# Optimization experiments

Hardware: AMD Instinct MI355X
Metric: run time of the kernel (lower is better)

Reference implementation:

```python
import jax, jax.numpy as jnp
import numpy as np

N = 100000   # num nodes
E = 500000   # num edges
F_IN = 128   # num_feats
H = 128      # dim_hidden
C = 40       # num_classes


def _glorot(key, fan_in, fan_out):
    lim = np.sqrt(6.0 / (fan_in + fan_out)).astype(np.float32)
    return jax.random.uniform(key, (fan_in, fan_out), jnp.float32, -lim, lim)


def setup_inputs() -> dict:
    key = jax.random.key(0)
    ks = jax.random.split(key, 8)
    x = jax.random.normal(ks[0], (N, F_IN), dtype=jnp.float32)
    edge_index = jax.random.randint(ks[1], (2, E), 0, N, dtype=jnp.int32)
    dims = [F_IN, H, H, H, C]  # num_layers = 4
    inp = {"x": x, "edge_index": edge_index}
    for i in range(4):
        inp[f"W{i}"] = _glorot(ks[2 + i], dims[i], dims[i + 1])
        inp[f"b{i}"] = jnp.zeros((dims[i + 1],), jnp.float32)
    return inp


def _gcn_norm(edge_index, num_nodes):
    # PyG gcn_norm: add self-loops (weight 1), symmetric D^-1/2 A D^-1/2
    loops = jnp.arange(num_nodes, dtype=edge_index.dtype)
    src = jnp.concatenate([edge_index[0], loops])
    dst = jnp.concatenate([edge_index[1], loops])
    deg = jax.ops.segment_sum(jnp.ones_like(src, jnp.float32), dst,
                              num_segments=num_nodes)
    dinv = jnp.where(deg > 0, jax.lax.rsqrt(deg), 0.0)
    norm = dinv[src] * dinv[dst]  # [E + N]
    return src, dst, norm


def _gcn_conv(h, W, b, src, dst, norm, num_nodes):
    h = h @ W                               # [N, out]
    msg = h[src] * norm[:, None]            # gather + scale, [E+N, out]
    agg = jax.ops.segment_sum(msg, dst, num_segments=num_nodes)
    return agg + b


def reference(x, edge_index, W0, b0, W1, b1, W2, b2, W3, b3):
    # eval mode: feature dropout and edge dropout (dropout_adj) are identity;
    # type_norm='None' -> no batchnorm.
    src, dst, norm = _gcn_norm(edge_index, N)
    Ws = [W0, W1, W2, W3]
    bs = [b0, b1, b2, b3]
    h = x
    for i in range(3):  # num_layers - 1 hidden layers with ReLU
        h = jax.nn.relu(_gcn_conv(h, Ws[i], bs[i], src, dst, norm, N))
    return _gcn_conv(h, Ws[3], bs[3], src, dst, norm, N)  # [N, C]
```

## Files before the change

### kernel.cpp

```cpp
#include <hip/hip_runtime.h>
#include <hip/hip_bf16.h>


#define F_DIM 128

#define SCAN_T 256
#define SCAN_I 8
#define SCAN_CHUNK (SCAN_T * SCAN_I)

typedef __attribute__((ext_vector_type(8))) short short8;
typedef __attribute__((ext_vector_type(4))) float f32x4;

__device__ __forceinline__ unsigned short f2bf_rne(float f) {
    unsigned int u = __float_as_uint(f);
    unsigned int r = (u + 0x7fffu + ((u >> 16) & 1u)) >> 16;
    return (unsigned short)r;
}

__global__ void count_dst_kernel(const int* __restrict__ dst, int* __restrict__ count, int E) {
    int e = blockIdx.x * blockDim.x + threadIdx.x;
    if (e < E) atomicAdd(&count[dst[e]], 1);
}

__global__ __launch_bounds__(SCAN_T) void scan_partial_kernel(const int* __restrict__ count,
                                                              int* __restrict__ blocksum, int n) {
    int b = blockIdx.x, t = threadIdx.x;
    int base = b * SCAN_CHUNK + t * SCAN_I;
    int s = 0;
#pragma unroll
    for (int j = 0; j < SCAN_I; ++j) {
        int i = base + j;
        if (i < n) s += count[i] + 1;
    }
    __shared__ int red[SCAN_T];
    red[t] = s;
    __syncthreads();
    for (int off = SCAN_T / 2; off > 0; off >>= 1) {
        if (t < off) red[t] += red[t + off];
        __syncthreads();
    }
    if (t == 0) blocksum[b] = red[0];
}

__global__ __launch_bounds__(1024) void scan_sums_kernel(const int* __restrict__ blocksum,
                                                         int* __restrict__ blockoff, int nb) {
    __shared__ int sums[1024];
    int t = threadIdx.x;
    sums[t] = (t < nb) ? blocksum[t] : 0;
    __syncthreads();
    for (int off = 1; off < 1024; off <<= 1) {
        int v = (t >= off) ? sums[t - off] : 0;
        __syncthreads();
        sums[t] += v;
        __syncthreads();
    }
    if (t < nb) blockoff[t] = (t == 0) ? 0 : sums[t - 1];
    if (t == 0) blockoff[nb] = sums[nb - 1];
}

__global__ __launch_bounds__(SCAN_T) void scan_write_fused_kernel(const int* __restrict__ count,
                                                                  const int* __restrict__ blockoff,
                                                                  int* __restrict__ rowptr,
                                                                  int* __restrict__ writepos,
                                                                  float* __restrict__ dinv,
                                                                  int* __restrict__ col,
                                                                  float* __restrict__ val,
                                                                  int n, int nb) {
    int b = blockIdx.x, t = threadIdx.x;
    int base = b * SCAN_CHUNK + t * SCAN_I;
    int c[SCAN_I];
    int s = 0;
#pragma unroll
    for (int j = 0; j < SCAN_I; ++j) {
        int i = base + j;
        c[j] = (i < n) ? count[i] + 1 : 0;
        s += c[j];
    }
    __shared__ int sums[SCAN_T];
    sums[t] = s;
    __syncthreads();
    for (int off = 1; off < SCAN_T; off <<= 1) {
        int v = (t >= off) ? sums[t - off] : 0;
        __syncthreads();
        sums[t] += v;
        __syncthreads();
    }
    int offset = blockoff[b] + ((t == 0) ? 0 : sums[t - 1]);
#pragma unroll
    for (int j = 0; j < SCAN_I; ++j) {
        int i = base + j;
        if (i < n) {
            rowptr[i] = offset;
            float d = rsqrtf((float)c[j]);
            dinv[i] = d;
            col[offset] = i;
            val[offset] = d * d;
            writepos[i] = offset + 1;
            offset += c[j];
        }
    }
    if (b == 0 && t == 0) rowptr[n] = blockoff[nb];
}

__global__ void fill_edges_kernel(const int* __restrict__ src, const int* __restrict__ dst,
                                  int* __restrict__ writepos, int* __restrict__ col,
                                  float* __restrict__ val, const float* __restrict__ dinv, int E) {
    int e = blockIdx.x * blockDim.x + threadIdx.x;
    if (e < E) {
        int s = src[e], d = dst[e];
        int p = atomicAdd(&writepos[d], 1);
        col[p] = s;
        val[p] = dinv[s] * dinv[d];
    }
}

__global__ __launch_bounds__(256) void cvt_bf16_kernel(const float* __restrict__ in,
                                                       unsigned short* __restrict__ out,
                                                       long nChunks) {
    long idx = (long)blockIdx.x * 256 + threadIdx.x;
    if (idx >= nChunks) return;
    const float4* in4 = (const float4*)in;
    float4 a = in4[idx * 2];
    float4 b = in4[idx * 2 + 1];
    uint4 o;
    o.x = (unsigned)f2bf_rne(a.x) | ((unsigned)f2bf_rne(a.y) << 16);
    o.y = (unsigned)f2bf_rne(a.z) | ((unsigned)f2bf_rne(a.w) << 16);
    o.z = (unsigned)f2bf_rne(b.x) | ((unsigned)f2bf_rne(b.y) << 16);
    o.w = (unsigned)f2bf_rne(b.z) | ((unsigned)f2bf_rne(b.w) << 16);
    ((uint4*)out)[idx] = o;
}

__global__ __launch_bounds__(256) void cvt_weights_kernel(const float* __restrict__ W0,
                                                          const float* __restrict__ W1,
                                                          const float* __restrict__ W2,
                                                          const float* __restrict__ W3,
                                                          unsigned short* __restrict__ WT0,
                                                          unsigned short* __restrict__ WT1,
                                                          unsigned short* __restrict__ WT2,
                                                          unsigned short* __restrict__ WT3) {
    int t = blockIdx.x * 256 + threadIdx.x;
    if (t < 3 * 16384) {
        int w = t >> 14, i = t & 16383;
        int k = i >> 7, c = i & 127;
        const float* W = (w == 0) ? W0 : (w == 1) ? W1 : W2;
        unsigned short* WT = (w == 0) ? WT0 : (w == 1) ? WT1 : WT2;
        WT[(size_t)c * 128 + k] = f2bf_rne(W[(size_t)k * 128 + c]);
    } else {
        int i = t - 3 * 16384;
        if (i < 48 * 128) {
            int c = i >> 7, k = i & 127;
            WT3[(size_t)c * 128 + k] = (c < 40) ? f2bf_rne(W3[(size_t)k * 40 + c])
                                                : (unsigned short)0;
        }
    }
}

__device__ __forceinline__ void acc8_bf16(float* acc, uint4 u, float v) {
    unsigned w[4] = {u.x, u.y, u.z, u.w};
#pragma unroll
    for (int i = 0; i < 4; ++i) {
        float lo = __uint_as_float(w[i] << 16);
        float hi = __uint_as_float(w[i] & 0xffff0000u);
        acc[2 * i] += v * lo;
        acc[2 * i + 1] += v * hi;
    }
}

__device__ __forceinline__ void gather_phase1(const int* __restrict__ rowptr,
                                              const int* __restrict__ col,
                                              const float* __restrict__ val,
                                              const uint4* __restrict__ H16,
                                              unsigned short (*aggb)[136], int n) {
    int m = threadIdx.x >> 3;
    int p = threadIdx.x & 7;
    int node = blockIdx.x * 32 + m;
    float acc[16];
#pragma unroll
    for (int q = 0; q < 16; ++q) acc[q] = 0.f;
    if (node < n) {
        int s = rowptr[node], e = rowptr[node + 1];
        int j = s;
        for (; j + 3 < e; j += 4) {
            int c0 = col[j], c1 = col[j + 1], c2 = col[j + 2], c3 = col[j + 3];
            float v0 = val[j], v1 = val[j + 1], v2 = val[j + 2], v3 = val[j + 3];
            const uint4* r0 = H16 + (size_t)c0 * 16 + p;
            const uint4* r1 = H16 + (size_t)c1 * 16 + p;
            const uint4* r2 = H16 + (size_t)c2 * 16 + p;
            const uint4* r3 = H16 + (size_t)c3 * 16 + p;
            uint4 a0 = r0[0], a1 = r0[8];
            uint4 b0 = r1[0], b1 = r1[8];
            uint4 g0 = r2[0], g1 = r2[8];
            uint4 d0 = r3[0], d1 = r3[8];
            acc8_bf16(acc + 0, a0, v0);
            acc8_bf16(acc + 8, a1, v0);
            acc8_bf16(acc + 0, b0, v1);
            acc8_bf16(acc + 8, b1, v1);
            acc8_bf16(acc + 0, g0, v2);
            acc8_bf16(acc + 8, g1, v2);
            acc8_bf16(acc + 0, d0, v3);
            acc8_bf16(acc + 8, d1, v3);
        }
        for (; j + 1 < e; j += 2) {
            int c0 = col[j], c1 = col[j + 1];
            float v0 = val[j], v1 = val[j + 1];
            const uint4* r0 = H16 + (size_t)c0 * 16 + p;
            const uint4* r1 = H16 + (size_t)c1 * 16 + p;
            uint4 a0 = r0[0], a1 = r0[8];
            uint4 b0 = r1[0], b1 = r1[8];
            acc8_bf16(acc + 0, a0, v0);
            acc8_bf16(acc + 8, a1, v0);
            acc8_bf16(acc + 0, b0, v1);
            acc8_bf16(acc + 8, b1, v1);
        }
        if (j < e) {
            int c0 = col[j];
            float v0 = val[j];
            const uint4* r0 = H16 + (size_t)c0 * 16 + p;
            uint4 a0 = r0[0], a1 = r0[8];
            acc8_bf16(acc + 0, a0, v0);
            acc8_bf16(acc + 8, a1, v0);
        }
    }
    short8 s0, s1;
#pragma unroll
    for (int q = 0; q < 8; ++q) s0[q] = (short)f2bf_rne(acc[q]);
#pragma unroll
    for (int q = 0; q < 8; ++q) s1[q] = (short)f2bf_rne(acc[8 + q]);
    *(short8*)&aggb[m][8 * p] = s0;
    *(short8*)&aggb[m][64 + 8 * p] = s1;
}

__global__ __launch_bounds__(256, 6) void fused_layer_mfma(const int* __restrict__ rowptr,
                                                           const int* __restrict__ col,
                                                           const float* __restrict__ val,
                                                           const unsigned short* __restrict__ Hin,
                                                           const unsigned short* __restrict__ WT,
                                                           const float* __restrict__ bias,
                                                           unsigned short* __restrict__ Hout,
                                                           int n) {
    __shared__ unsigned short aggb[32][136];
    gather_phase1(rowptr, col, val, (const uint4*)Hin, aggb, n);
    __syncthreads();

    int lane = threadIdx.x & 63;
    int wv = threadIdx.x >> 6;
    int l15 = lane & 15;
    int lg = lane >> 4;

    f32x4 a00 = {0.f, 0.f, 0.f, 0.f}, a01 = a00, a10 = a00, a11 = a00;

#pragma unroll
    for (int kc = 0; kc < 4; ++kc) {
        int ko = kc * 32 + lg * 8;
        short8 fa0 = *(const short8*)&aggb[l15][ko];
        short8 fa1 = *(const short8*)&aggb[l15 + 16][ko];
        short8 fb0 = *(const short8*)&WT[(size_t)(wv * 32 + l15) * 128 + ko];
        short8 fb1 = *(const short8*)&WT[(size_t)(wv * 32 + 16 + l15) * 128 + ko];
        a00 = __builtin_amdgcn_mfma_f32_16x16x32_bf16(fa0, fb0, a00, 0, 0, 0);
        a01 = __builtin_amdgcn_mfma_f32_16x16x32_bf16(fa0, fb1, a01, 0, 0, 0);
        a10 = __builtin_amdgcn_mfma_f32_16x16x32_bf16(fa1, fb0, a10, 0, 0, 0);
        a11 = __builtin_amdgcn_mfma_f32_16x16x32_bf16(fa1, fb1, a11, 0, 0, 0);
    }

    int base = blockIdx.x * 32;
#pragma unroll
    for (int nt = 0; nt < 2; ++nt) {
        int c = wv * 32 + nt * 16 + l15;
        float bv = bias[c];
#pragma unroll
        for (int mt = 0; mt < 2; ++mt) {
            f32x4 acc = (mt == 0) ? (nt == 0 ? a00 : a01) : (nt == 0 ? a10 : a11);
#pragma unroll
            for (int r = 0; r < 4; ++r) {
                int node = base + mt * 16 + lg * 4 + r;
                if (node < n) {
                    float o = fmaxf(acc[r] + bv, 0.f);
                    Hout[(size_t)node * 128 + c] = f2bf_rne(o);
                }
            }
        }
    }
}

__global__ __launch_bounds__(256, 6) void fused_layer_mfma_w3(const int* __restrict__ rowptr,
                                                              const int* __restrict__ col,
                                                              const float* __restrict__ val,
                                                              const unsigned short* __restrict__ Hin,
                                                              const unsigned short* __restrict__ WT,
                                                              const float* __restrict__ bias,
                                                              const unsigned short* __restrict__ WT3,
                                                              unsigned short* __restrict__ hw3,
                                                              int n) {
    __shared__ unsigned short aggb[32][136];
    gather_phase1(rowptr, col, val, (const uint4*)Hin, aggb, n);
    __syncthreads();

    int lane = threadIdx.x & 63;
    int wv = threadIdx.x >> 6;
    int l15 = lane & 15;
    int lg = lane >> 4;

    f32x4 a00 = {0.f, 0.f, 0.f, 0.f}, a01 = a00, a10 = a00, a11 = a00;

#pragma unroll
    for (int kc = 0; kc < 4; ++kc) {
        int ko = kc * 32 + lg * 8;
        short8 fa0 = *(const short8*)&aggb[l15][ko];
        short8 fa1 = *(const short8*)&aggb[l15 + 16][ko];
        short8 fb0 = *(const short8*)&WT[(size_t)(wv * 32 + l15) * 128 + ko];
        short8 fb1 = *(const short8*)&WT[(size_t)(wv * 32 + 16 + l15) * 128 + ko];
        a00 = __builtin_amdgcn_mfma_f32_16x16x32_bf16(fa0, fb0, a00, 0, 0, 0);
        a01 = __builtin_amdgcn_mfma_f32_16x16x32_bf16(fa0, fb1, a01, 0, 0, 0);
        a10 = __builtin_amdgcn_mfma_f32_16x16x32_bf16(fa1, fb0, a10, 0, 0, 0);
        a11 = __builtin_amdgcn_mfma_f32_16x16x32_bf16(fa1, fb1, a11, 0, 0, 0);
    }

    __syncthreads();
#pragma unroll
    for (int nt = 0; nt < 2; ++nt) {
        int c = wv * 32 + nt * 16 + l15;
        float bv = bias[c];
#pragma unroll
        for (int mt = 0; mt < 2; ++mt) {
            f32x4 acc = (mt == 0) ? (nt == 0 ? a00 : a01) : (nt == 0 ? a10 : a11);
#pragma unroll
            for (int r = 0; r < 4; ++r) {
                int row = mt * 16 + lg * 4 + r;
                aggb[row][c] = f2bf_rne(fmaxf(acc[r] + bv, 0.f));
            }
        }
    }
    __syncthreads();

    if (wv < 3) {
        f32x4 c0 = {0.f, 0.f, 0.f, 0.f}, c1 = c0;
#pragma unroll
        for (int kc = 0; kc < 4; ++kc) {
            int ko = kc * 32 + lg * 8;
            short8 fa0 = *(const short8*)&aggb[l15][ko];
            short8 fa1 = *(const short8*)&aggb[l15 + 16][ko];
            short8 fb = *(const short8*)&WT3[(size_t)(wv * 16 + l15) * 128 + ko];
            c0 = __builtin_amdgcn_mfma_f32_16x16x32_bf16(fa0, fb, c0, 0, 0, 0);
            c1 = __builtin_amdgcn_mfma_f32_16x16x32_bf16(fa1, fb, c1, 0, 0, 0);
        }
        int ccol = wv * 16 + l15;
        if (ccol < 40) {
            int base = blockIdx.x * 32;
#pragma unroll
            for (int mt = 0; mt < 2; ++mt) {
                f32x4 acc = (mt == 0) ? c0 : c1;
#pragma unroll
                for (int r = 0; r < 4; ++r) {
                    int node = base + mt * 16 + lg * 4 + r;
                    if (node < n) hw3[(size_t)node * 40 + ccol] = f2bf_rne(acc[r]);
                }
            }
        }
    }
}

__global__ __launch_bounds__(256, 8) void gather40_bf16_kernel(const int* __restrict__ rowptr,
                                                               const int* __restrict__ col,
                                                               const float* __restrict__ val,
                                                               const unsigned short* __restrict__ hw3,
                                                               const float* __restrict__ bias,
                                                               float* __restrict__ out, int n) {
    int m = threadIdx.x >> 3;
    int p = threadIdx.x & 7;
    int node = blockIdx.x * 32 + m;
    if (node >= n) return;

    float a0x = 0.f, a0y = 0.f, a0z = 0.f, a0w = 0.f;
    float a1x = 0.f, a1y = 0.f, a1z = 0.f, a1w = 0.f;

    int s = rowptr[node], e = rowptr[node + 1];
    int j = s;
    for (; j + 1 < e; j += 2) {
        int c0 = col[j], c1 = col[j + 1];
        float v0 = val[j], v1 = val[j + 1];
        const uint2* r0 = (const uint2*)(hw3 + (size_t)c0 * 40);
        const uint2* r1 = (const uint2*)(hw3 + (size_t)c1 * 40);
        uint2 u0 = r0[p], u1 = r1[p];
        a0x += v0 * __uint_as_float(u0.x << 16) + v1 * __uint_as_float(u1.x << 16);
        a0y += v0 * __uint_as_float(u0.x & 0xffff0000u) + v1 * __uint_as_float(u1.x & 0xffff0000u);
        a0z += v0 * __uint_as_float(u0.y << 16) + v1 * __uint_as_float(u1.y << 16);
        a0w += v0 * __uint_as_float(u0.y & 0xffff0000u) + v1 * __uint_as_float(u1.y & 0xffff0000u);
        if (p < 2) {
            uint2 w0 = r0[8 + p], w1 = r1[8 + p];
            a1x += v0 * __uint_as_float(w0.x << 16) + v1 * __uint_as_float(w1.x << 16);
            a1y += v0 * __uint_as_float(w0.x & 0xffff0000u) + v1 * __uint_as_float(w1.x & 0xffff0000u);
            a1z += v0 * __uint_as_float(w0.y << 16) + v1 * __uint_as_float(w1.y << 16);
            a1w += v0 * __uint_as_float(w0.y & 0xffff0000u) + v1 * __uint_as_float(w1.y & 0xffff0000u);
        }
    }
    if (j < e) {
        int c0 = col[j];
        float v0 = val[j];
        const uint2* r0 = (const uint2*)(hw3 + (size_t)c0 * 40);
        uint2 u = r0[p];
        a0x += v0 * __uint_as_float(u.x << 16);
        a0y += v0 * __uint_as_float(u.x & 0xffff0000u);
        a0z += v0 * __uint_as_float(u.y << 16);
        a0w += v0 * __uint_as_float(u.y & 0xffff0000u);
        if (p < 2) {
            uint2 w = r0[8 + p];
            a1x += v0 * __uint_as_float(w.x << 16);
            a1y += v0 * __uint_as_float(w.x & 0xffff0000u);
            a1z += v0 * __uint_as_float(w.y << 16);
            a1w += v0 * __uint_as_float(w.y & 0xffff0000u);
        }
    }

    const float4* bi = (const float4*)bias;
    float4 bv = bi[p];
    float4 o0;
    o0.x = a0x + bv.x; o0.y = a0y + bv.y;
    o0.z = a0z + bv.z; o0.w = a0w + bv.w;
    ((float4*)(out + (size_t)node * 40))[p] = o0;
    if (p < 2) {
        float4 bw = bi[8 + p];
        float4 o1;
        o1.x = a1x + bw.x; o1.y = a1y + bw.y;
        o1.z = a1z + bw.z; o1.w = a1w + bw.w;
        ((float4*)(out + (size_t)node * 40))[8 + p] = o1;
    }
}

extern "C" void kernel_launch(void* const* d_in, const int* in_sizes, int n_in,
                              void* d_out, int out_size, void* d_ws, size_t ws_size,
                              hipStream_t stream) {
    const float* x = (const float*)d_in[0];
    const int* edge_index = (const int*)d_in[1];
    const float* W0 = (const float*)d_in[2];
    const float* b0 = (const float*)d_in[3];
    const float* W1 = (const float*)d_in[4];
    const float* b1 = (const float*)d_in[5];
    const float* W2 = (const float*)d_in[6];
    const float* b2 = (const float*)d_in[7];
    const float* W3 = (const float*)d_in[8];
    const float* b3 = (const float*)d_in[9];

    const int E = in_sizes[1] / 2;
    const int N = in_sizes[0] / F_DIM;
    const int NNZ = E + N;
    const int NB = (N + SCAN_CHUNK - 1) / SCAN_CHUNK;

    const int* src = edge_index;
    const int* dst = edge_index + E;

    char* ws = (char*)d_ws;
    size_t off = 0;
    auto carve = [&](size_t bytes) -> void* {
        void* p = ws + off;
        off = (off + bytes + 255) & ~(size_t)255;
        return p;
    };
    unsigned short* hbA = (unsigned short*)carve((size_t)N * F_DIM * sizeof(unsigned short));
    unsigned short* hbB = (unsigned short*)carve((size_t)N * F_DIM * sizeof(unsigned short));
    unsigned short* hw3 = (unsigned short*)carve((size_t)N * 40 * sizeof(unsigned short));
    unsigned short* WT0 = (unsigned short*)carve(128 * 128 * sizeof(unsigned short));
    unsigned short* WT1 = (unsigned short*)carve(128 * 128 * sizeof(unsigned short));
    unsigned short* WT2 = (unsigned short*)carve(128 * 128 * sizeof(unsigned short));
    unsigned short* WT3 = (unsigned short*)carve(48 * 128 * sizeof(unsigned short));
    int* count = (int*)carve((size_t)N * sizeof(int));
    float* dinv = (float*)carve((size_t)N * sizeof(float));
    int* rowptr = (int*)carve((size_t)(N + 1) * sizeof(int));
    int* writepos = (int*)carve((size_t)N * sizeof(int));
    int* colbuf = (int*)carve((size_t)NNZ * sizeof(int));
    float* valbuf = (float*)carve((size_t)NNZ * sizeof(float));
    int* blocksum = (int*)carve((size_t)NB * sizeof(int));
    int* blockoff = (int*)carve((size_t)(NB + 1) * sizeof(int));
    (void)ws_size;

    hipMemsetAsync(count, 0, (size_t)N * sizeof(int), stream);
    count_dst_kernel<<<(E + 255) / 256, 256, 0, stream>>>(dst, count, E);
    {
        long nChunks = (long)N * F_DIM / 8;
        cvt_bf16_kernel<<<(int)((nChunks + 255) / 256), 256, 0, stream>>>(x, hbA, nChunks);
    }
    cvt_weights_kernel<<<(3 * 16384 + 48 * 128 + 255) / 256, 256, 0, stream>>>(
        W0, W1, W2, W3, WT0, WT1, WT2, WT3);
    scan_partial_kernel<<<NB, SCAN_T, 0, stream>>>(count, blocksum, N);
    scan_sums_kernel<<<1, 1024, 0, stream>>>(blocksum, blockoff, NB);
    scan_write_fused_kernel<<<NB, SCAN_T, 0, stream>>>(count, blockoff, rowptr, writepos,
                                                       dinv, colbuf, valbuf, N, NB);
    fill_edges_kernel<<<(E + 255) / 256, 256, 0, stream>>>(src, dst, writepos, colbuf, valbuf, dinv, E);

    int nblk32 = (N + 31) / 32;
    fused_layer_mfma<<<nblk32, 256, 0, stream>>>(rowptr, colbuf, valbuf, hbA, WT0, b0, hbB, N);
    fused_layer_mfma<<<nblk32, 256, 0, stream>>>(rowptr, colbuf, valbuf, hbB, WT1, b1, hbA, N);
    fused_layer_mfma_w3<<<nblk32, 256, 0, stream>>>(rowptr, colbuf, valbuf, hbA, WT2, b2, WT3, hw3, N);

    gather40_bf16_kernel<<<nblk32, 256, 0, stream>>>(rowptr, colbuf, valbuf, hw3, b3, (float*)d_out, N);
}
```

Measured before the change: 257.5 us.

## Merge preprocessing kernels, drop 4-way gather unroll, raise occupancy bound to 8

Three independent preprocessing kernels (degree counting, feature bf16 conversion, weight transpose/convert) are merged into one launch that picks its role from the block index, removing two launch gaps. The 4-edge unrolled gather loop is removed so the gather runs 2 edges at a time, and the launch-bounds minimum blocks per CU on the fused layer kernels rises from 6 to 8. Together these lower register pressure and raise occupancy, trading per-thread memory-level parallelism for more resident waves. The tighter register budget could also cause spills.

```diff
diff --git a/kernel.cpp b/kernel.cpp
--- a/kernel.cpp
+++ b/kernel.cpp
@@ -17,9 +17,54 @@
     return (unsigned short)r;
 }
 
-__global__ void count_dst_kernel(const int* __restrict__ dst, int* __restrict__ count, int E) {
-    int e = blockIdx.x * blockDim.x + threadIdx.x;
-    if (e < E) atomicAdd(&count[dst[e]], 1);
+__global__ __launch_bounds__(256) void preproc_kernel(const int* __restrict__ dst,
+                                                      int* __restrict__ count, int E,
+                                                      const float* __restrict__ x,
+                                                      unsigned short* __restrict__ xb,
+                                                      long nChunks,
+                                                      const float* __restrict__ W0,
+                                                      const float* __restrict__ W1,
+                                                      const float* __restrict__ W2,
+                                                      const float* __restrict__ W3,
+                                                      unsigned short* __restrict__ WT0,
+                                                      unsigned short* __restrict__ WT1,
+                                                      unsigned short* __restrict__ WT2,
+                                                      unsigned short* __restrict__ WT3,
+                                                      int EB, int XB) {
+    int b = blockIdx.x;
+    if (b < EB) {
+        int e = b * 256 + threadIdx.x;
+        if (e < E) atomicAdd(&count[dst[e]], 1);
+    } else if (b < EB + XB) {
+        long idx = (long)(b - EB) * 256 + threadIdx.x;
+        if (idx < nChunks) {
+            const float4* in4 = (const float4*)x;
+            float4 a = in4[idx * 2];
+            float4 c = in4[idx * 2 + 1];
+            uint4 o;
+            o.x = (unsigned)f2bf_rne(a.x) | ((unsigned)f2bf_rne(a.y) << 16);
+            o.y = (unsigned)f2bf_rne(a.z) | ((unsigned)f2bf_rne(a.w) << 16);
+            o.z = (unsigned)f2bf_rne(c.x) | ((unsigned)f2bf_rne(c.y) << 16);
+            o.w = (unsigned)f2bf_rne(c.z) | ((unsigned)f2bf_rne(c.w) << 16);
+            ((uint4*)xb)[idx] = o;
+        }
+    } else {
+        int t = (b - EB - XB) * 256 + threadIdx.x;
+        if (t < 3 * 16384) {
+            int w = t >> 14, i = t & 16383;
+            int k = i >> 7, c = i & 127;
+            const float* W = (w == 0) ? W0 : (w == 1) ? W1 : W2;
+            unsigned short* WT = (w == 0) ? WT0 : (w == 1) ? WT1 : WT2;
+            WT[(size_t)c * 128 + k] = f2bf_rne(W[(size_t)k * 128 + c]);
+        } else {
+            int i = t - 3 * 16384;
+            if (i < 48 * 128) {
+                int c = i >> 7, k = i & 127;
+                WT3[(size_t)c * 128 + k] = (c < 40) ? f2bf_rne(W3[(size_t)k * 40 + c])
+                                                    : (unsigned short)0;
+            }
+        }
+    }
 }
 
 __global__ __launch_bounds__(SCAN_T) void scan_partial_kernel(const int* __restrict__ count,
@@ -114,47 +159,6 @@
     }
 }
 
-__global__ __launch_bounds__(256) void cvt_bf16_kernel(const float* __restrict__ in,
-                                                       unsigned short* __restrict__ out,
-                                                       long nChunks) {
-    long idx = (long)blockIdx.x * 256 + threadIdx.x;
-    if (idx >= nChunks) return;
-    const float4* in4 = (const float4*)in;
-    float4 a = in4[idx * 2];
-    float4 b = in4[idx * 2 + 1];
-    uint4 o;
-    o.x = (unsigned)f2bf_rne(a.x) | ((unsigned)f2bf_rne(a.y) << 16);
-    o.y = (unsigned)f2bf_rne(a.z) | ((unsigned)f2bf_rne(a.w) << 16);
-    o.z = (unsigned)f2bf_rne(b.x) | ((unsigned)f2bf_rne(b.y) << 16);
-    o.w = (unsigned)f2bf_rne(b.z) | ((unsigned)f2bf_rne(b.w) << 16);
-    ((uint4*)out)[idx] = o;
-}
-
-__global__ __launch_bounds__(256) void cvt_weights_kernel(const float* __restrict__ W0,
-                                                          const float* __restrict__ W1,
-                                                          const float* __restrict__ W2,
-                                                          const float* __restrict__ W3,
-                                                          unsigned short* __restrict__ WT0,
-                                                          unsigned short* __restrict__ WT1,
-                                                          unsigned short* __restrict__ WT2,
-                                                          unsigned short* __restrict__ WT3) {
-    int t = blockIdx.x * 256 + threadIdx.x;
-    if (t < 3 * 16384) {
-        int w = t >> 14, i = t & 16383;
-        int k = i >> 7, c = i & 127;
-        const float* W = (w == 0) ? W0 : (w == 1) ? W1 : W2;
-        unsigned short* WT = (w == 0) ? WT0 : (w == 1) ? WT1 : WT2;
-        WT[(size_t)c * 128 + k] = f2bf_rne(W[(size_t)k * 128 + c]);
-    } else {
-        int i = t - 3 * 16384;
-        if (i < 48 * 128) {
-            int c = i >> 7, k = i & 127;
-            WT3[(size_t)c * 128 + k] = (c < 40) ? f2bf_rne(W3[(size_t)k * 40 + c])
-                                                : (unsigned short)0;
-        }
-    }
-}
-
 __device__ __forceinline__ void acc8_bf16(float* acc, uint4 u, float v) {
     unsigned w[4] = {u.x, u.y, u.z, u.w};
 #pragma unroll
@@ -180,26 +184,6 @@
     if (node < n) {
         int s = rowptr[node], e = rowptr[node + 1];
         int j = s;
-        for (; j + 3 < e; j += 4) {
-            int c0 = col[j], c1 = col[j + 1], c2 = col[j + 2], c3 = col[j + 3];
-            float v0 = val[j], v1 = val[j + 1], v2 = val[j + 2], v3 = val[j + 3];
-            const uint4* r0 = H16 + (size_t)c0 * 16 + p;
-            const uint4* r1 = H16 + (size_t)c1 * 16 + p;
-            const uint4* r2 = H16 + (size_t)c2 * 16 + p;
-            const uint4* r3 = H16 + (size_t)c3 * 16 + p;
-            uint4 a0 = r0[0], a1 = r0[8];
-            uint4 b0 = r1[0], b1 = r1[8];
-            uint4 g0 = r2[0], g1 = r2[8];
-            uint4 d0 = r3[0], d1 = r3[8];
-            acc8_bf16(acc + 0, a0, v0);
-            acc8_bf16(acc + 8, a1, v0);
-            acc8_bf16(acc + 0, b0, v1);
-            acc8_bf16(acc + 8, b1, v1);
-            acc8_bf16(acc + 0, g0, v2);
-            acc8_bf16(acc + 8, g1, v2);
-            acc8_bf16(acc + 0, d0, v3);
-            acc8_bf16(acc + 8, d1, v3);
-        }
         for (; j + 1 < e; j += 2) {
             int c0 = col[j], c1 = col[j + 1];
             float v0 = val[j], v1 = val[j + 1];
@@ -230,7 +214,7 @@
     *(short8*)&aggb[m][64 + 8 * p] = s1;
 }
 
-__global__ __launch_bounds__(256, 6) void fused_layer_mfma(const int* __restrict__ rowptr,
+__global__ __launch_bounds__(256, 8) void fused_layer_mfma(const int* __restrict__ rowptr,
                                                            const int* __restrict__ col,
                                                            const float* __restrict__ val,
                                                            const unsigned short* __restrict__ Hin,
@@ -282,7 +266,7 @@
     }
 }
 
-__global__ __launch_bounds__(256, 6) void fused_layer_mfma_w3(const int* __restrict__ rowptr,
+__global__ __launch_bounds__(256, 8) void fused_layer_mfma_w3(const int* __restrict__ rowptr,
                                                               const int* __restrict__ col,
                                                               const float* __restrict__ val,
                                                               const unsigned short* __restrict__ Hin,
@@ -473,13 +457,15 @@
     (void)ws_size;
 
     hipMemsetAsync(count, 0, (size_t)N * sizeof(int), stream);
-    count_dst_kernel<<<(E + 255) / 256, 256, 0, stream>>>(dst, count, E);
     {
         long nChunks = (long)N * F_DIM / 8;
-        cvt_bf16_kernel<<<(int)((nChunks + 255) / 256), 256, 0, stream>>>(x, hbA, nChunks);
-    }
-    cvt_weights_kernel<<<(3 * 16384 + 48 * 128 + 255) / 256, 256, 0, stream>>>(
-        W0, W1, W2, W3, WT0, WT1, WT2, WT3);
+        int EB = (E + 255) / 256;
+        int XB = (int)((nChunks + 255) / 256);
+        int WB = (3 * 16384 + 48 * 128 + 255) / 256;
+        preproc_kernel<<<EB + XB + WB, 256, 0, stream>>>(dst, count, E, x, hbA, nChunks,
+                                                         W0, W1, W2, W3, WT0, WT1, WT2, WT3,
+                                                         EB, XB);
+    }
     scan_partial_kernel<<<NB, SCAN_T, 0, stream>>>(count, blocksum, N);
     scan_sums_kernel<<<1, 1024, 0, stream>>>(blocksum, blockoff, NB);
     scan_write_fused_kernel<<<NB, SCAN_T, 0, stream>>>(count, blockoff, rowptr, writepos,
```

After: 228.9 us. -11.1%, faster.
